# Kernel tuning notes

Hardware: AMD Instinct MI355X
Metric: run time of the kernel (lower is better)

The kernel has to match this reference:

```python
import jax, jax.numpy as jnp
import numpy as np

H = 512  # hidden_dim
T = 12   # pred_seq_len
D_OUT = 2


def setup_inputs() -> dict:
    key = jax.random.key(0)
    ks = jax.random.split(key, 13)
    s = lambda fan: 1.0 / np.sqrt(fan)
    return {
        "z":    jax.random.normal(ks[0], (4096, 128), jnp.float32),
        "x":    jax.random.normal(ks[1], (4096, 128), jnp.float32),
        "x_0":  jax.random.normal(ks[2], (4096, 4), jnp.float32),
        "W_ia": jax.random.normal(ks[3], (2, 4), jnp.float32) * s(4),
        "b_ia": jax.random.normal(ks[4], (2,), jnp.float32) * s(4),
        "W_h0": jax.random.normal(ks[5], (H, 256), jnp.float32) * s(256),
        "b_h0": jax.random.normal(ks[6], (H,), jnp.float32) * s(256),
        "W_ih": jax.random.normal(ks[7], (3 * H, 258), jnp.float32) * s(H),
        "b_ih": jax.random.normal(ks[8], (3 * H,), jnp.float32) * s(H),
        "W_hh": jax.random.normal(ks[9], (3 * H, H), jnp.float32) * s(H),
        "b_hh": jax.random.normal(ks[10], (3 * H,), jnp.float32) * s(H),
        "W_out": jax.random.normal(ks[11], (D_OUT, H), jnp.float32) * s(H),
        "b_out": jax.random.normal(ks[12], (D_OUT,), jnp.float32) * s(H),
        "num_samples": 1,
    }


def _gru_cell(inp, h, W_ih, b_ih, W_hh, b_hh):
    # torch.nn.GRUCell math
    gi = inp @ W_ih.T + b_ih  # [N, 3H]
    gh = h @ W_hh.T + b_hh    # [N, 3H]
    gi_r, gi_z, gi_n = jnp.split(gi, 3, axis=-1)
    gh_r, gh_z, gh_n = jnp.split(gh, 3, axis=-1)
    r = jax.nn.sigmoid(gi_r + gh_r)
    u = jax.nn.sigmoid(gi_z + gh_z)
    n = jnp.tanh(gi_n + r * gh_n)
    return (1.0 - u) * n + u * h


def reference(z, x, x_0, W_ia, b_ia, W_h0, b_h0, W_ih, b_ih, W_hh, b_hh, W_out, b_out, num_samples):
    zx = jnp.concatenate([z, x], axis=-1)          # [N, 256]
    h0 = zx @ W_h0.T + b_h0                        # [N, H]
    a0 = x_0 @ W_ia.T + b_ia                       # [N, 2] initial action

    def step(carry, _):
        h, x_t = carry
        inp = jnp.concatenate([zx, x_t], axis=-1)  # [N, 258]
        h_new = _gru_cell(inp, h, W_ih, b_ih, W_hh, b_hh)
        out = h_new @ W_out.T + b_out              # [N, 2]
        # sample_traj with 'mse' loss: deterministic mean
        return (h_new, out), out

    (_, _), outs = jax.lax.scan(step, (h0, a0), None, length=T)  # outs: [T, N, 2]
    N = z.shape[0]
    outs = outs.reshape(T, num_samples, N // num_samples, D_OUT)
    return jnp.transpose(outs, (1, 2, 0, 3))       # [S, B, T, 2]
```

## Files before the change

### kernel.cpp

```cpp
#include <hip/hip_runtime.h>
#include <cstdint>
#include <cstddef>


typedef __attribute__((ext_vector_type(8))) _Float16 f16x8;
typedef __attribute__((ext_vector_type(4))) float floatx4;

__device__ unsigned g_cnt[8 * 64];
__device__ unsigned g_gbar[16 * 64];

__device__ __align__(256) _Float16 g_h[12][16 * 16 * 256 * 32];
__device__ __align__(256) float    g_P[12][16 * 16 * 512];

__device__ __forceinline__ float sigm_f(float v) { return 1.0f / (1.0f + __expf(-v)); }
__device__ __forceinline__ float tanh_f(float v) { return 2.0f / (1.0f + __expf(-2.0f * v)) - 1.0f; }

__device__ __forceinline__ void async16(void* lds, const void* g) {
    __builtin_amdgcn_global_load_lds(
        (const __attribute__((address_space(1))) void*)g,
        (__attribute__((address_space(3))) void*)lds, 16, 0, 0);
}

__device__ __forceinline__ f16x8 ldzx8(const float* __restrict__ z,
                                       const float* __restrict__ x,
                                       int i, int c) {
    const float* s = (c < 128) ? (z + (size_t)i * 128 + c)
                               : (x + (size_t)i * 128 + (c - 128));
    float4 a = ((const float4*)s)[0], b = ((const float4*)s)[1];
    return (f16x8){(_Float16)a.x, (_Float16)a.y, (_Float16)a.z, (_Float16)a.w,
                   (_Float16)b.x, (_Float16)b.y, (_Float16)b.z, (_Float16)b.w};
}

__device__ __forceinline__ void group_barrier16(unsigned gidx) {
    asm volatile("s_waitcnt vmcnt(0)" ::: "memory");
    __syncthreads();
    if (threadIdx.x == 0) {
        unsigned* ctr = &g_gbar[gidx * 64];
        unsigned t = __hip_atomic_fetch_add(ctr, 1u, __ATOMIC_RELAXED,
                                            __HIP_MEMORY_SCOPE_AGENT);
        unsigned target = (t & ~15u) + 16u;
        while (__hip_atomic_load(ctr, __ATOMIC_RELAXED,
                                 __HIP_MEMORY_SCOPE_AGENT) < target)
            __builtin_amdgcn_s_sleep(1);
    }
    __syncthreads();
}

__global__ __launch_bounds__(512, 1) void k_all(
    const float* __restrict__ z, const float* __restrict__ x,
    const float* __restrict__ x0, const float* __restrict__ W_ia,
    const float* __restrict__ b_ia, const float* __restrict__ W_h0,
    const float* __restrict__ b_h0, const float* __restrict__ W_ih,
    const float* __restrict__ b_ih, const float* __restrict__ W_hh,
    const float* __restrict__ b_hh, const float* __restrict__ W_out,
    const float* __restrict__ b_out, float* __restrict__ dout)
{
    extern __shared__ __align__(16) char smem[];
    const uint32_t BOFF = 0, HST = 98304, XSO = 114688, DOUT = 116736,
                   DUM = 141312, SLO = 142336;
    const int tid = threadIdx.x;
    float* xs = (float*)(smem + XSO);
    float* douts = (float*)(smem + DOUT);

    unsigned xcc;
    asm volatile("s_getreg_b32 %0, hwreg(HW_REG_XCC_ID)" : "=s"(xcc));
    xcc &= 7u;
    if (tid == 0) {
        unsigned s = __hip_atomic_fetch_add(&g_cnt[xcc * 64], 1u, __ATOMIC_RELAXED,
                                            __HIP_MEMORY_SCOPE_AGENT) & 31u;
        *(unsigned*)(smem + SLO) = s;
    }
    __syncthreads();
    const unsigned slot = *(volatile unsigned*)(smem + SLO);
    const int shalf = slot >> 4, cgrp = slot & 15;
    const unsigned gidx = xcc * 2 + shalf;
    const int M0g = (int)gidx * 256;
    const int jc0 = cgrp * 32;

    const int wv = tid >> 6, lane = tid & 63;
    const int l15 = lane & 15, q2 = lane >> 4;

    if (wv == 0) {
        const char* wb = (const char*)&g_h[0][0] + (size_t)gidx * 262144 +
                         (size_t)cgrp * 16384 + (size_t)lane * 128;
        async16(smem + DUM, wb);
        async16(smem + DUM, wb + 8192);
    }
    if (wv == 1) {
        const char* wp = (const char*)&g_P[0][0] +
                         ((size_t)gidx * 8192 + (size_t)cgrp * 512) * 4 +
                         (size_t)(lane & 15) * 128;
        async16(smem + DUM, wp);
    }

    #pragma unroll
    for (int u = 0; u < 8; u++) {
        int sl2 = u * 512 + tid;
        int r = sl2 >> 5, s = sl2 & 31;
        int c = (s ^ (r & 15)) << 3;
        f16x8 v;
        if (r < 96) {
            int nrow = (r >> 5) * 512 + jc0 + (r & 31);
            const float2* src = (const float2*)(W_ih + (size_t)nrow * 258 + c);
            float2 a0 = src[0], a1 = src[1], a2 = src[2], a3 = src[3];
            v = (f16x8){(_Float16)a0.x, (_Float16)a0.y, (_Float16)a1.x, (_Float16)a1.y,
                        (_Float16)a2.x, (_Float16)a2.y, (_Float16)a3.x, (_Float16)a3.y};
        } else {
            int nrow = jc0 + (r - 96);
            const float4* src = (const float4*)(W_h0 + (size_t)nrow * 256 + c);
            float4 a = src[0], b = src[1];
            v = (f16x8){(_Float16)a.x, (_Float16)a.y, (_Float16)a.z, (_Float16)a.w,
                        (_Float16)b.x, (_Float16)b.y, (_Float16)b.z, (_Float16)b.w};
        }
        *(f16x8*)(smem + (uint32_t)(r * 512 + s * 16)) = v;
    }

    float4 p0v[2], p1v[2], p2v[2]; float wo0[2], wo1[2];
    float bih[3][2], bh0[2];
    #pragma unroll
    for (int jt = 0; jt < 2; jt++) {
        int jc = jc0 + jt * 16 + l15;
        p0v[jt] = make_float4(W_ih[(size_t)jc * 258 + 256],
                              W_ih[(size_t)jc * 258 + 257],
                              W_ih[(size_t)(512 + jc) * 258 + 256],
                              W_ih[(size_t)(512 + jc) * 258 + 257]);
        p1v[jt] = make_float4(W_ih[(size_t)(1024 + jc) * 258 + 256],
                              W_ih[(size_t)(1024 + jc) * 258 + 257],
                              b_hh[jc], b_hh[512 + jc]);
        p2v[jt] = make_float4(b_hh[1024 + jc], W_out[jc], W_out[512 + jc], 0.f);
        wo0[jt] = p2v[jt].y; wo1[jt] = p2v[jt].z;
        bh0[jt] = b_h0[jc];
        #pragma unroll
        for (int g = 0; g < 3; g++) bih[g][jt] = b_ih[g * 512 + jc];
    }
    const float bo = b_out[lane & 1];
    const float bia_d = b_ia[lane & 1];
    float4 wia_d = make_float4(W_ia[(lane & 1) * 4 + 0], W_ia[(lane & 1) * 4 + 1],
                               W_ia[(lane & 1) * 4 + 2], W_ia[(lane & 1) * 4 + 3]);

    uint32_t bbase[6];
    #pragma unroll
    for (int g = 0; g < 3; g++)
        #pragma unroll
        for (int jt = 0; jt < 2; jt++) {
            int r = g * 32 + jt * 16 + l15;
            bbase[g * 2 + jt] = BOFF + (uint32_t)r * 1024 +
                                ((uint32_t)(q2 ^ (r & 3)) << 4) +
                                ((uint32_t)((r >> 2) & 3) << 6);
        }
    uint32_t pb[8];
    #pragma unroll
    for (int sl = 0; sl < 8; sl++) {
        int r = (sl < 6) ? ((sl >> 1) * 32 + (sl & 1) * 16 + l15)
                         : (96 + (sl - 6) * 16 + l15);
        pb[sl] = BOFF + (uint32_t)r * 512 +
                 ((uint32_t)(q2 ^ (r & 3)) << 4) +
                 ((uint32_t)((r >> 2) & 3) << 6);
    }
    __syncthreads();

    const int ia0 = M0g + (wv * 2 + 0) * 16 + l15;
    const int ia1 = M0g + (wv * 2 + 1) * 16 + l15;
    floatx4 accP[2][8];
    #pragma unroll
    for (int mt = 0; mt < 2; mt++)
        #pragma unroll
        for (int sl = 0; sl < 8; sl++) accP[mt][sl] = (floatx4){0.f, 0.f, 0.f, 0.f};
    {
        f16x8 aq[4][2];
        #define ALOADZ(S, KS) do { \
            aq[S][0] = ldzx8(z, x, ia0, (KS) * 32 + q2 * 8); \
            aq[S][1] = ldzx8(z, x, ia1, (KS) * 32 + q2 * 8); \
        } while (0)
        ALOADZ(0, 0); ALOADZ(1, 1); ALOADZ(2, 2);
        #pragma unroll
        for (int ks = 0; ks < 8; ks++) {
            if (ks < 5) { ALOADZ((ks + 3) & 3, ks + 3); }
            f16x8 a0 = aq[ks & 3][0];
            f16x8 a1 = aq[ks & 3][1];
            const uint32_t kadd = (uint32_t)((ks >> 2) << 8);
            const uint32_t kxor = (uint32_t)((ks & 3) << 6);
            #pragma unroll
            for (int sl = 0; sl < 8; sl++) {
                f16x8 b = *(const f16x8*)(smem + ((pb[sl] + kadd) ^ kxor));
                accP[0][sl] = __builtin_amdgcn_mfma_f32_16x16x32_f16(a0, b, accP[0][sl], 0, 0, 0);
                accP[1][sl] = __builtin_amdgcn_mfma_f32_16x16x32_f16(a1, b, accP[1][sl], 0, 0, 0);
            }
        }
        #undef ALOADZ
    }

    float gi[2][3][2][4];
    #pragma unroll
    for (int mt = 0; mt < 2; mt++)
        #pragma unroll
        for (int g = 0; g < 3; g++)
            #pragma unroll
            for (int jt = 0; jt < 2; jt++)
                #pragma unroll
                for (int reg = 0; reg < 4; reg++)
                    gi[mt][g][jt][reg] = accP[mt][g * 2 + jt][reg] + bih[g][jt];
    #pragma unroll
    for (int mt = 0; mt < 2; mt++)
        #pragma unroll
        for (int jt = 0; jt < 2; jt++)
            #pragma unroll
            for (int reg = 0; reg < 4; reg++) {
                int rl = (wv * 2 + mt) * 16 + q2 * 4 + reg;
                float v = accP[mt][6 + jt][reg] + bh0[jt];
                *(_Float16*)(smem + HST + (uint32_t)(rl * 64 + (jt * 16 + l15) * 2)) = (_Float16)v;
            }
    __syncthreads();

    #pragma unroll
    for (int u = 0; u < 12; u++) {
        int sl2 = u * 512 + tid;
        int r = sl2 >> 6, l = sl2 & 63;
        int nrow = (r >> 5) * 512 + jc0 + (r & 31);
        int c = (l ^ (r & 15)) << 3;
        const float4* src = (const float4*)(W_hh + (size_t)nrow * 512 + c);
        float4 a = src[0], b = src[1];
        f16x8 v = {(_Float16)a.x, (_Float16)a.y, (_Float16)a.z, (_Float16)a.w,
                   (_Float16)b.x, (_Float16)b.y, (_Float16)b.z, (_Float16)b.w};
        *(f16x8*)(smem + (uint32_t)(r * 1024 + l * 16)) = v;
    }
    {
        int row = tid >> 1, half = tid & 1;
        const char* sl = smem + HST + (uint32_t)(row * 64 + half * 32);
        char* gd = (char*)&g_h[0][0] + (size_t)gidx * 262144 + (size_t)cgrp * 16384 +
                   (size_t)row * 64 + (size_t)half * 32;
        *(f16x8*)gd = *(const f16x8*)sl;
        *(f16x8*)(gd + 16) = *(const f16x8*)(sl + 16);
    }
    group_barrier16(gidx);

    #pragma unroll 1
    for (int t = 0; t < 12; t++) {
        float pv[16];
        if (t > 0) {
            const float* pbase = &g_P[t - 1][0] + (size_t)gidx * 8192 +
                                 (size_t)(wv * 32 + (lane >> 1)) * 2 + (size_t)(lane & 1);
            #pragma unroll
            for (int c = 0; c < 16; c++) pv[c] = pbase[c * 512];
        }

        if (t < 11 && wv == 0) {
            const char* wb = (const char*)&g_h[t + 1][0] + (size_t)gidx * 262144 +
                             (size_t)cgrp * 16384 + (size_t)lane * 128;
            async16(smem + DUM, wb);
            async16(smem + DUM, wb + 8192);
        }
        if (wv == 1) {
            const char* wp = (const char*)&g_P[t][0] +
                             ((size_t)gidx * 8192 + (size_t)cgrp * 512) * 4 +
                             (size_t)(lane & 15) * 128;
            async16(smem + DUM, wp);
        }

        const char* hb = (const char*)&g_h[t][0] + (size_t)gidx * 262144 + (size_t)q2 * 16;
        const char* rp0 = hb + (size_t)((wv * 2 + 0) * 16 + l15) * 64;
        const char* rp1 = hb + (size_t)((wv * 2 + 1) * 16 + l15) * 64;
        floatx4 acc[2][3][2];
        #pragma unroll
        for (int mt = 0; mt < 2; mt++)
            #pragma unroll
            for (int g = 0; g < 3; g++)
                #pragma unroll
                for (int jt = 0; jt < 2; jt++)
                    acc[mt][g][jt] = (floatx4){0.f, 0.f, 0.f, 0.f};

        f16x8 aq[8][2];
        #define ALOAD(S, KS) do { \
            aq[S][0] = *(const f16x8*)(rp0 + (size_t)(KS) * 16384); \
            aq[S][1] = *(const f16x8*)(rp1 + (size_t)(KS) * 16384); \
        } while (0)
        ALOAD(0, 0); ALOAD(1, 1); ALOAD(2, 2); ALOAD(3, 3);
        ALOAD(4, 4); ALOAD(5, 5); ALOAD(6, 6); ALOAD(7, 7);

        #pragma unroll
        for (int ks = 0; ks < 16; ks++) {
            f16x8 a0 = aq[ks & 7][0];
            f16x8 a1 = aq[ks & 7][1];
            if (ks < 8) { ALOAD(ks & 7, ks + 8); }
            const uint32_t kadd = (uint32_t)((ks >> 2) << 8);
            const uint32_t kxor = (uint32_t)((ks & 3) << 6);
            #pragma unroll
            for (int g = 0; g < 3; g++)
                #pragma unroll
                for (int jt = 0; jt < 2; jt++) {
                    f16x8 b = *(const f16x8*)(smem + ((bbase[g * 2 + jt] + kadd) ^ kxor));
                    acc[0][g][jt] = __builtin_amdgcn_mfma_f32_16x16x32_f16(a0, b, acc[0][g][jt], 0, 0, 0);
                    acc[1][g][jt] = __builtin_amdgcn_mfma_f32_16x16x32_f16(a1, b, acc[1][g][jt], 0, 0, 0);
                }
        }
        #undef ALOAD

        {
            float v;
            if (t == 0) {
                int i = M0g + wv * 32 + (lane >> 1);
                float4 xr = *(const float4*)(x0 + (size_t)i * 4);
                v = bia_d + xr.x * wia_d.x + xr.y * wia_d.y +
                            xr.z * wia_d.z + xr.w * wia_d.w;
            } else {
                v = bo;
                #pragma unroll
                for (int c = 0; c < 16; c++) v += pv[c];
                douts[wv * 768 + (t - 1) * 64 + lane] = v;
            }
            xs[wv * 64 + lane] = v;
        }

        #pragma unroll
        for (int mt = 0; mt < 2; mt++) {
            float po[4][2];
            #pragma unroll
            for (int reg = 0; reg < 4; reg++) { po[reg][0] = 0.f; po[reg][1] = 0.f; }
            #pragma unroll
            for (int jt = 0; jt < 2; jt++) {
                #pragma unroll
                for (int reg = 0; reg < 4; reg++) {
                    int local = mt * 16 + q2 * 4 + reg;
                    int rl = wv * 32 + local;
                    float2 xv = *(const float2*)(smem + XSO + (uint32_t)((wv * 64 + local * 2) * 4));
                    _Float16* hp = (_Float16*)(smem + HST + (uint32_t)(rl * 64 + (jt * 16 + l15) * 2));
                    float hold = (float)hp[0];
                    float r  = sigm_f(gi[mt][0][jt][reg] + p0v[jt].x * xv.x + p0v[jt].y * xv.y + acc[mt][0][jt][reg] + p1v[jt].z);
                    float u  = sigm_f(gi[mt][1][jt][reg] + p0v[jt].z * xv.x + p0v[jt].w * xv.y + acc[mt][1][jt][reg] + p1v[jt].w);
                    float nn = tanh_f(gi[mt][2][jt][reg] + p1v[jt].x * xv.x + p1v[jt].y * xv.y + r * (acc[mt][2][jt][reg] + p2v[jt].x));
                    float hn = (1.f - u) * nn + u * hold;
                    hp[0] = (_Float16)hn;
                    po[reg][0] += hn * wo0[jt];
                    po[reg][1] += hn * wo1[jt];
                }
            }
            #pragma unroll
            for (int m = 1; m < 16; m <<= 1)
                #pragma unroll
                for (int reg = 0; reg < 4; reg++) {
                    po[reg][0] += __shfl_xor(po[reg][0], m);
                    po[reg][1] += __shfl_xor(po[reg][1], m);
                }
            if (l15 == 0) {
                #pragma unroll
                for (int reg = 0; reg < 4; reg++) {
                    int local = mt * 16 + q2 * 4 + reg;
                    float* pp = &g_P[t][0] + (size_t)gidx * 8192 + (size_t)cgrp * 512 +
                                (size_t)(wv * 32 + local) * 2;
                    *(float2*)pp = make_float2(po[reg][0], po[reg][1]);
                }
            }
        }

        if (t < 11) {
            int rloc = wv * 32 + (lane >> 1);
            int half = lane & 1;
            const char* sl = smem + HST + (uint32_t)(rloc * 64 + half * 32);
            char* gd = (char*)&g_h[t + 1][0] + (size_t)gidx * 262144 +
                       (size_t)cgrp * 16384 + (size_t)rloc * 64 + (size_t)half * 32;
            *(f16x8*)gd = *(const f16x8*)sl;
            *(f16x8*)(gd + 16) = *(const f16x8*)(sl + 16);
        }
        group_barrier16(gidx);
    }

    if (cgrp == 0) {
        const float* pbase = &g_P[11][0] + (size_t)gidx * 8192 +
                             (size_t)(wv * 32 + (lane >> 1)) * 2 + (size_t)(lane & 1);
        float v = bo;
        #pragma unroll
        for (int c = 0; c < 16; c++) v += pbase[c * 512];
        douts[wv * 768 + 11 * 64 + lane] = v;
        size_t i = (size_t)(M0g + wv * 32 + (lane >> 1));
        int d = lane & 1;
        #pragma unroll
        for (int t = 0; t < 12; t++)
            dout[(i * 12 + t) * 2 + d] = douts[wv * 768 + t * 64 + lane];
    }
}

extern "C" void kernel_launch(void* const* d_in, const int* in_sizes, int n_in,
                              void* d_out, int out_size, void* d_ws, size_t ws_size,
                              hipStream_t stream)
{
    const float* z     = (const float*)d_in[0];
    const float* x     = (const float*)d_in[1];
    const float* x0    = (const float*)d_in[2];
    const float* W_ia  = (const float*)d_in[3];
    const float* b_ia  = (const float*)d_in[4];
    const float* W_h0  = (const float*)d_in[5];
    const float* b_h0  = (const float*)d_in[6];
    const float* W_ih  = (const float*)d_in[7];
    const float* b_ih  = (const float*)d_in[8];
    const float* W_hh  = (const float*)d_in[9];
    const float* b_hh  = (const float*)d_in[10];
    const float* W_out = (const float*)d_in[11];
    const float* b_out = (const float*)d_in[12];
    float* dout = (float*)d_out;

    static bool s_attr_done = false;
    if (!s_attr_done) {
        hipFuncSetAttribute((const void*)k_all,
                            hipFuncAttributeMaxDynamicSharedMemorySize, 142400);
        s_attr_done = true;
    }

    k_all<<<256, 512, 142400, stream>>>(z, x, x0, W_ia, b_ia, W_h0, b_h0,
                                        W_ih, b_ih, W_hh, b_hh, W_out, b_out,
                                        dout);
}
```

Measured before the change: 274.4 us.

## Double-buffer cross-block hidden state and partials, pipeline loads with explicit waitcnt

Replaces the 12-slot global buffers for hidden state and output partials with ping-pong buffers, so the working set is small and can stay cache-resident. The per-step A-operand loads become inline-asm global loads with sc0, issued three stages ahead through a 4-deep register ring with hand-placed vmcnt waits, and the partial-output loads are issued alongside them. The per-step async prefetch-to-dummy-LDS warming is removed; instead the prologue warms both buffers. The risk is that the fixed vmcnt counts and the two-buffer reuse depend on exact load ordering and on the group barrier for correctness.

```diff
diff --git a/kernel.cpp b/kernel.cpp
--- a/kernel.cpp
+++ b/kernel.cpp
@@ -9,8 +9,8 @@
 __device__ unsigned g_cnt[8 * 64];
 __device__ unsigned g_gbar[16 * 64];
 
-__device__ __align__(256) _Float16 g_h[12][16 * 16 * 256 * 32];
-__device__ __align__(256) float    g_P[12][16 * 16 * 512];
+__device__ __align__(256) _Float16 g_h2[2][16 * 16 * 256 * 32];
+__device__ __align__(256) float    g_P2[2][16 * 16 * 512];
 
 __device__ __forceinline__ float sigm_f(float v) { return 1.0f / (1.0f + __expf(-v)); }
 __device__ __forceinline__ float tanh_f(float v) { return 2.0f / (1.0f + __expf(-2.0f * v)) - 1.0f; }
@@ -21,14 +21,11 @@
         (__attribute__((address_space(3))) void*)lds, 16, 0, 0);
 }
 
-__device__ __forceinline__ f16x8 ldzx8(const float* __restrict__ z,
-                                       const float* __restrict__ x,
-                                       int i, int c) {
-    const float* s = (c < 128) ? (z + (size_t)i * 128 + c)
-                               : (x + (size_t)i * 128 + (c - 128));
-    float4 a = ((const float4*)s)[0], b = ((const float4*)s)[1];
-    return (f16x8){(_Float16)a.x, (_Float16)a.y, (_Float16)a.z, (_Float16)a.w,
-                   (_Float16)b.x, (_Float16)b.y, (_Float16)b.z, (_Float16)b.w};
+__device__ __forceinline__ void aload16(f16x8& d, const char* p) {
+    asm volatile("global_load_dwordx4 %0, %1, off sc0" : "=&v"(d) : "v"(p));
+}
+__device__ __forceinline__ void pload4(float& d, const float* p) {
+    asm volatile("global_load_dword %0, %1, off sc0" : "=&v"(d) : "v"(p));
 }
 
 __device__ __forceinline__ void group_barrier16(unsigned gidx) {
@@ -44,6 +41,16 @@
             __builtin_amdgcn_s_sleep(1);
     }
     __syncthreads();
+}
+
+__device__ __forceinline__ f16x8 ldzx8(const float* __restrict__ z,
+                                       const float* __restrict__ x,
+                                       int i, int c) {
+    const float* s = (c < 128) ? (z + (size_t)i * 128 + c)
+                               : (x + (size_t)i * 128 + (c - 128));
+    float4 a = ((const float4*)s)[0], b = ((const float4*)s)[1];
+    return (f16x8){(_Float16)a.x, (_Float16)a.y, (_Float16)a.z, (_Float16)a.w,
+                   (_Float16)b.x, (_Float16)b.y, (_Float16)b.z, (_Float16)b.w};
 }
 
 __global__ __launch_bounds__(512, 1) void k_all(
@@ -81,13 +88,25 @@
     const int l15 = lane & 15, q2 = lane >> 4;
 
     if (wv == 0) {
-        const char* wb = (const char*)&g_h[0][0] + (size_t)gidx * 262144 +
+        const char* wb = (const char*)&g_h2[0][0] + (size_t)gidx * 262144 +
                          (size_t)cgrp * 16384 + (size_t)lane * 128;
         async16(smem + DUM, wb);
         async16(smem + DUM, wb + 8192);
     }
     if (wv == 1) {
-        const char* wp = (const char*)&g_P[0][0] +
+        const char* wb = (const char*)&g_h2[1][0] + (size_t)gidx * 262144 +
+                         (size_t)cgrp * 16384 + (size_t)lane * 128;
+        async16(smem + DUM, wb);
+        async16(smem + DUM, wb + 8192);
+    }
+    if (wv == 2) {
+        const char* wp = (const char*)&g_P2[0][0] +
+                         ((size_t)gidx * 8192 + (size_t)cgrp * 512) * 4 +
+                         (size_t)(lane & 15) * 128;
+        async16(smem + DUM, wp);
+    }
+    if (wv == 3) {
+        const char* wp = (const char*)&g_P2[1][0] +
                          ((size_t)gidx * 8192 + (size_t)cgrp * 512) * 4 +
                          (size_t)(lane & 15) * 128;
         async16(smem + DUM, wp);
@@ -167,17 +186,17 @@
         #pragma unroll
         for (int sl = 0; sl < 8; sl++) accP[mt][sl] = (floatx4){0.f, 0.f, 0.f, 0.f};
     {
-        f16x8 aq[4][2];
+        f16x8 aqz[4][2];
         #define ALOADZ(S, KS) do { \
-            aq[S][0] = ldzx8(z, x, ia0, (KS) * 32 + q2 * 8); \
-            aq[S][1] = ldzx8(z, x, ia1, (KS) * 32 + q2 * 8); \
+            aqz[S][0] = ldzx8(z, x, ia0, (KS) * 32 + q2 * 8); \
+            aqz[S][1] = ldzx8(z, x, ia1, (KS) * 32 + q2 * 8); \
         } while (0)
         ALOADZ(0, 0); ALOADZ(1, 1); ALOADZ(2, 2);
         #pragma unroll
         for (int ks = 0; ks < 8; ks++) {
             if (ks < 5) { ALOADZ((ks + 3) & 3, ks + 3); }
-            f16x8 a0 = aq[ks & 3][0];
-            f16x8 a1 = aq[ks & 3][1];
+            f16x8 a0 = aqz[ks & 3][0];
+            f16x8 a1 = aqz[ks & 3][1];
             const uint32_t kadd = (uint32_t)((ks >> 2) << 8);
             const uint32_t kxor = (uint32_t)((ks & 3) << 6);
             #pragma unroll
@@ -227,7 +246,7 @@
     {
         int row = tid >> 1, half = tid & 1;
         const char* sl = smem + HST + (uint32_t)(row * 64 + half * 32);
-        char* gd = (char*)&g_h[0][0] + (size_t)gidx * 262144 + (size_t)cgrp * 16384 +
+        char* gd = (char*)&g_h2[0][0] + (size_t)gidx * 262144 + (size_t)cgrp * 16384 +
                    (size_t)row * 64 + (size_t)half * 32;
         *(f16x8*)gd = *(const f16x8*)sl;
         *(f16x8*)(gd + 16) = *(const f16x8*)(sl + 16);
@@ -236,28 +255,16 @@
 
     #pragma unroll 1
     for (int t = 0; t < 12; t++) {
-        float pv[16];
-        if (t > 0) {
-            const float* pbase = &g_P[t - 1][0] + (size_t)gidx * 8192 +
-                                 (size_t)(wv * 32 + (lane >> 1)) * 2 + (size_t)(lane & 1);
-            #pragma unroll
-            for (int c = 0; c < 16; c++) pv[c] = pbase[c * 512];
-        }
-
-        if (t < 11 && wv == 0) {
-            const char* wb = (const char*)&g_h[t + 1][0] + (size_t)gidx * 262144 +
-                             (size_t)cgrp * 16384 + (size_t)lane * 128;
-            async16(smem + DUM, wb);
-            async16(smem + DUM, wb + 8192);
-        }
-        if (wv == 1) {
-            const char* wp = (const char*)&g_P[t][0] +
-                             ((size_t)gidx * 8192 + (size_t)cgrp * 512) * 4 +
-                             (size_t)(lane & 15) * 128;
-            async16(smem + DUM, wp);
-        }
-
-        const char* hb = (const char*)&g_h[t][0] + (size_t)gidx * 262144 + (size_t)q2 * 16;
+        if (t == 0) {
+            int i = M0g + wv * 32 + (lane >> 1);
+            float4 xr = *(const float4*)(x0 + (size_t)i * 4);
+            float v = bia_d + xr.x * wia_d.x + xr.y * wia_d.y +
+                      xr.z * wia_d.z + xr.w * wia_d.w;
+            xs[wv * 64 + lane] = v;
+        }
+
+        const char* hb = (const char*)&g_h2[t & 1][0] + (size_t)gidx * 262144 +
+                         (size_t)q2 * 16;
         const char* rp0 = hb + (size_t)((wv * 2 + 0) * 16 + l15) * 64;
         const char* rp1 = hb + (size_t)((wv * 2 + 1) * 16 + l15) * 64;
         floatx4 acc[2][3][2];
@@ -269,19 +276,31 @@
                 for (int jt = 0; jt < 2; jt++)
                     acc[mt][g][jt] = (floatx4){0.f, 0.f, 0.f, 0.f};
 
-        f16x8 aq[8][2];
-        #define ALOAD(S, KS) do { \
-            aq[S][0] = *(const f16x8*)(rp0 + (size_t)(KS) * 16384); \
-            aq[S][1] = *(const f16x8*)(rp1 + (size_t)(KS) * 16384); \
+        f16x8 aq[4][2];
+        #define AISS(S, KS) do { \
+            aload16(aq[S][0], rp0 + (size_t)(KS) * 16384); \
+            aload16(aq[S][1], rp1 + (size_t)(KS) * 16384); \
         } while (0)
-        ALOAD(0, 0); ALOAD(1, 1); ALOAD(2, 2); ALOAD(3, 3);
-        ALOAD(4, 4); ALOAD(5, 5); ALOAD(6, 6); ALOAD(7, 7);
+        AISS(0, 0); AISS(1, 1); AISS(2, 2);
+
+        float pv[16];
+        {
+            const float* pbase = &g_P2[(t + 1) & 1][0] + (size_t)gidx * 8192 +
+                                 (size_t)(wv * 32 + (lane >> 1)) * 2 + (size_t)(lane & 1);
+            #pragma unroll
+            for (int c = 0; c < 16; c++) pload4(pv[c], pbase + c * 512);
+        }
 
         #pragma unroll
         for (int ks = 0; ks < 16; ks++) {
-            f16x8 a0 = aq[ks & 7][0];
-            f16x8 a1 = aq[ks & 7][1];
-            if (ks < 8) { ALOAD(ks & 7, ks + 8); }
+            if (ks < 3)        asm volatile("s_waitcnt vmcnt(20)" ::: "memory");
+            else if (ks < 14)  asm volatile("s_waitcnt vmcnt(4)"  ::: "memory");
+            else if (ks == 14) asm volatile("s_waitcnt vmcnt(2)"  ::: "memory");
+            else               asm volatile("s_waitcnt vmcnt(0)"  ::: "memory");
+            __builtin_amdgcn_sched_barrier(0);
+            f16x8 a0 = aq[ks & 3][0];
+            f16x8 a1 = aq[ks & 3][1];
+            if (ks < 13) { AISS((ks + 3) & 3, ks + 3); }
             const uint32_t kadd = (uint32_t)((ks >> 2) << 8);
             const uint32_t kxor = (uint32_t)((ks & 3) << 6);
             #pragma unroll
@@ -293,21 +312,13 @@
                     acc[1][g][jt] = __builtin_amdgcn_mfma_f32_16x16x32_f16(a1, b, acc[1][g][jt], 0, 0, 0);
                 }
         }
-        #undef ALOAD
-
-        {
-            float v;
-            if (t == 0) {
-                int i = M0g + wv * 32 + (lane >> 1);
-                float4 xr = *(const float4*)(x0 + (size_t)i * 4);
-                v = bia_d + xr.x * wia_d.x + xr.y * wia_d.y +
-                            xr.z * wia_d.z + xr.w * wia_d.w;
-            } else {
-                v = bo;
-                #pragma unroll
-                for (int c = 0; c < 16; c++) v += pv[c];
-                douts[wv * 768 + (t - 1) * 64 + lane] = v;
-            }
+        #undef AISS
+
+        if (t > 0) {
+            float v = bo;
+            #pragma unroll
+            for (int c = 0; c < 16; c++) v += pv[c];
+            douts[wv * 768 + (t - 1) * 64 + lane] = v;
             xs[wv * 64 + lane] = v;
         }
 
@@ -345,7 +356,7 @@
                 #pragma unroll
                 for (int reg = 0; reg < 4; reg++) {
                     int local = mt * 16 + q2 * 4 + reg;
-                    float* pp = &g_P[t][0] + (size_t)gidx * 8192 + (size_t)cgrp * 512 +
+                    float* pp = &g_P2[t & 1][0] + (size_t)gidx * 8192 + (size_t)cgrp * 512 +
                                 (size_t)(wv * 32 + local) * 2;
                     *(float2*)pp = make_float2(po[reg][0], po[reg][1]);
                 }
@@ -356,7 +367,7 @@
             int rloc = wv * 32 + (lane >> 1);
             int half = lane & 1;
             const char* sl = smem + HST + (uint32_t)(rloc * 64 + half * 32);
-            char* gd = (char*)&g_h[t + 1][0] + (size_t)gidx * 262144 +
+            char* gd = (char*)&g_h2[(t + 1) & 1][0] + (size_t)gidx * 262144 +
                        (size_t)cgrp * 16384 + (size_t)rloc * 64 + (size_t)half * 32;
             *(f16x8*)gd = *(const f16x8*)sl;
             *(f16x8*)(gd + 16) = *(const f16x8*)(sl + 16);
@@ -365,11 +376,16 @@
     }
 
     if (cgrp == 0) {
-        const float* pbase = &g_P[11][0] + (size_t)gidx * 8192 +
+        float pv[16];
+        const float* pbase = &g_P2[1][0] + (size_t)gidx * 8192 +
                              (size_t)(wv * 32 + (lane >> 1)) * 2 + (size_t)(lane & 1);
+        #pragma unroll
+        for (int c = 0; c < 16; c++) pload4(pv[c], pbase + c * 512);
+        asm volatile("s_waitcnt vmcnt(0)" ::: "memory");
+        __builtin_amdgcn_sched_barrier(0);
         float v = bo;
         #pragma unroll
-        for (int c = 0; c < 16; c++) v += pbase[c * 512];
+        for (int c = 0; c < 16; c++) v += pv[c];
         douts[wv * 768 + 11 * 64 + lane] = v;
         size_t i = (size_t)(M0g + wv * 32 + (lane >> 1));
         int d = lane & 1;
```

New measurement: 225.5 us. -17.8%, faster.
